# Optimization experiments

Hardware: AMD Instinct MI355X
Metric: run time of the kernel (lower is better)

The kernel has to match this reference:

```python
import jax, jax.numpy as jnp
import numpy as np

C = 1024
HEAD = 128

def setup_inputs() -> dict:
    key = jax.random.key(0)
    kx, kq, kk, kv = jax.random.split(key, 4)
    x = jax.random.normal(kx, (8, 2048, C), dtype=jnp.float32)
    s = 1.0 / np.sqrt(C)
    Wq = jax.random.normal(kq, (C, HEAD), dtype=jnp.float32) * s
    Wk = jax.random.normal(kk, (C, HEAD), dtype=jnp.float32) * s
    Wv = jax.random.normal(kv, (C, HEAD), dtype=jnp.float32) * s
    return {"x": x, "Wq": Wq, "Wk": Wk, "Wv": Wv}

def reference(x, Wq, Wk, Wv):
    B, T, Cdim = x.shape
    q = jnp.einsum('btc,ch->bth', x, Wq)
    k = jnp.einsum('btc,ch->bth', x, Wk)
    v = jnp.einsum('btc,ch->bth', x, Wv)
    # scores scaled by C**-0.5 (faithful to source, which uses input width C)
    wei = jnp.einsum('bqh,bkh->bqk', q, k) * (Cdim ** -0.5)
    causal = jnp.tril(jnp.ones((T, T), dtype=bool))
    wei = jnp.where(causal, wei, -jnp.inf)
    wei = jax.nn.softmax(wei, axis=-1)
    # dropout p=0.0 -> identity
    return jnp.einsum('bqk,bkh->bqh', wei, v)
```

## Files before the change

### kernel.cpp

```cpp
#include <hip/hip_runtime.h>
#include <hip/hip_bf16.h>


typedef __attribute__((ext_vector_type(8))) short bf16x8;
typedef __attribute__((ext_vector_type(4))) float f32x4;

#define NB   8
#define TT   2048
#define CDIM 1024
#define HD   128
#define NTOK (NB * TT)
#define NW   384

using bf16 = __hip_bfloat16;

__device__ __forceinline__ short f2bs(float f) {
    unsigned u = __builtin_bit_cast(unsigned, f);
    return (short)((u + 0x7FFF + ((u >> 16) & 1)) >> 16);
}

__global__ __launch_bounds__(256) void prep_w_kernel(
        const float* __restrict__ Wq, const float* __restrict__ Wk,
        const float* __restrict__ Wv, bf16* __restrict__ Wp) {
    const int f  = blockIdx.x * 256 + threadIdx.x;
    const int l  = f & 63;
    const int nt = (f >> 6) % 24;
    const int sl = f / 1536;
    const int ln = l & 15, quad = l >> 4;
    const int n  = nt * 16 + ln;
    const int w  = n >> 7, h = n & 127;
    const float* W = (w == 0) ? Wq : (w == 1) ? Wk : Wv;
    const int k0 = sl * 32 + quad * 8;
    bf16x8 frag;
    #pragma unroll
    for (int j = 0; j < 8; j++)
        frag[j] = f2bs(W[(long)(k0 + j) * HD + h]);
    *(bf16x8*)((short*)Wp + (long)f * 8) = frag;
}

__global__ __launch_bounds__(512, 4) void qkv_proj_kernel(
        const float* __restrict__ x, const bf16* __restrict__ Wp,
        bf16* __restrict__ Q, bf16* __restrict__ Kp, bf16* __restrict__ Vp) {
    __shared__ __align__(16) short aLDS[2 * 32 * 64 * 8];
    const int tid  = threadIdx.x;
    const int wave = tid >> 6, lane = tid & 63;
    const int quad = lane >> 4, ln = lane & 15;
    const long mbase = (long)blockIdx.x * 32;

    #pragma unroll
    for (int j = 0; j < 8; j++) {
        const int fid = j * 512 + tid;
        const int fl  = fid & 63;
        const int fsl = (fid >> 6) & 31;
        const int fmt = fid >> 11;
        const float4* src = (const float4*)(
            x + (mbase + fmt * 16 + (fl & 15)) * CDIM + fsl * 32 + (fl >> 4) * 8);
        float4 u = src[0], v = src[1];
        bf16x8 fr;
        fr[0] = f2bs(u.x); fr[1] = f2bs(u.y); fr[2] = f2bs(u.z); fr[3] = f2bs(u.w);
        fr[4] = f2bs(v.x); fr[5] = f2bs(v.y); fr[6] = f2bs(v.z); fr[7] = f2bs(v.w);
        *(bf16x8*)(aLDS + (long)fid * 8) = fr;
    }
    __syncthreads();

    const f32x4 zero = {0.f, 0.f, 0.f, 0.f};
    f32x4 acc[2][3];
    #pragma unroll
    for (int mt = 0; mt < 2; mt++)
        #pragma unroll
        for (int nt = 0; nt < 3; nt++) acc[mt][nt] = zero;

    const short* a0 = aLDS + lane * 8;
    const short* bp = (const short*)Wp + (long)wave * 1536 + lane * 8;

    #pragma unroll 4
    for (int sl = 0; sl < 32; sl++) {
        bf16x8 af0 = *(const bf16x8*)(a0 + sl * 512);
        bf16x8 af1 = *(const bf16x8*)(a0 + 16384 + sl * 512);
        bf16x8 b0  = *(const bf16x8*)(bp + (long)sl * 12288);
        bf16x8 b1  = *(const bf16x8*)(bp + (long)sl * 12288 + 512);
        bf16x8 b2  = *(const bf16x8*)(bp + (long)sl * 12288 + 1024);
        acc[0][0] = __builtin_amdgcn_mfma_f32_16x16x32_bf16(af0, b0, acc[0][0], 0, 0, 0);
        acc[0][1] = __builtin_amdgcn_mfma_f32_16x16x32_bf16(af0, b1, acc[0][1], 0, 0, 0);
        acc[0][2] = __builtin_amdgcn_mfma_f32_16x16x32_bf16(af0, b2, acc[0][2], 0, 0, 0);
        acc[1][0] = __builtin_amdgcn_mfma_f32_16x16x32_bf16(af1, b0, acc[1][0], 0, 0, 0);
        acc[1][1] = __builtin_amdgcn_mfma_f32_16x16x32_bf16(af1, b1, acc[1][1], 0, 0, 0);
        acc[1][2] = __builtin_amdgcn_mfma_f32_16x16x32_bf16(af1, b2, acc[1][2], 0, 0, 0);
    }

    __syncthreads();
    short* kT = aLDS;
    short* vT = aLDS + 8192;

    #pragma unroll
    for (int mt = 0; mt < 2; mt++) {
        #pragma unroll
        for (int nt = 0; nt < 3; nt++) {
            const int n = wave * 48 + nt * 16 + ln;
            #pragma unroll
            for (int r = 0; r < 4; r++) {
                const int row = mt * 16 + quad * 4 + r;
                const short hv = f2bs(acc[mt][nt][r]);
                if (n < 128) {
                    long g = mbase + row;
                    int b = (int)(g >> 11), t = (int)(g & (TT - 1));
                    Q[((long)b * TT + t) * HD + n] = __builtin_bit_cast(bf16, hv);
                } else if (n < 256) {
                    kT[row * 136 + (n - 128)] = hv;
                } else {
                    vT[(n - 256) * 40 + row] = hv;
                }
            }
        }
    }
    __syncthreads();

    {
        const long tile = blockIdx.x;
        const int  kc = wave >> 1, ntk = wave & 1;
        bf16x8 kv = *(const bf16x8*)&kT[(ntk*16 + ln)*136 + kc*32 + quad*8];
        *(bf16x8*)((short*)Kp + (tile*8 + wave)*512 + lane*8) = kv;
        bf16x8 vv = *(const bf16x8*)&vT[(wave*16 + ln)*40 + quad*8];
        *(bf16x8*)((short*)Vp + (tile*8 + wave)*512 + lane*8) = vv;
    }
}

__global__ __launch_bounds__(256, 2) void attn_kernel(
        const bf16* __restrict__ Q, const bf16* __restrict__ Kp,
        const bf16* __restrict__ Vp, float* __restrict__ out) {
    __shared__ __align__(16) char smem[33024];

    const int tid  = threadIdx.x;
    const int wave = tid >> 6, lane = tid & 63;
    const int quad = lane >> 4, ln = lane & 15;
    const int b   = blockIdx.x & 7;
    const int idx = blockIdx.x >> 3;
    const int qi  = (idx >> 5) ? (idx & 31) : 63 - (idx & 31);
    const int qb  = qi * 32;
    const int ntiles = qi + 1;
    const int t0 = (ntiles * wave) >> 2;
    const int t1 = (ntiles * (wave + 1)) >> 2;

    const bf16*  Qb  = Q + (long)b * TT * HD;
    const short* Kpb = (const short*)Kp + (long)b * 64 * 4096;
    const short* Vpb = (const short*)Vp + (long)b * 64 * 4096;

    short* pwave = (short*)smem + wave * 2560;

    bf16x8 qf[2][4];
    #pragma unroll
    for (int mt = 0; mt < 2; mt++)
        #pragma unroll
        for (int kc = 0; kc < 4; kc++)
            qf[mt][kc] = *(const bf16x8*)(Qb + (long)(qb + mt*16 + ln)*HD + kc*32 + quad*8);

    const f32x4 zero = {0.f, 0.f, 0.f, 0.f};
    f32x4 o[2][8];
    #pragma unroll
    for (int mt = 0; mt < 2; mt++)
        #pragma unroll
        for (int ht = 0; ht < 8; ht++) o[mt][ht] = zero;
    float li[2][4] = {{0.f,0.f,0.f,0.f},{0.f,0.f,0.f,0.f}};

    for (int kt = t0; kt < t1; ++kt) {
        const int j0 = kt * 32;
        const short* kbase = Kpb + (long)kt * 4096 + lane * 8;
        bf16x8 kf[4][2];
        #pragma unroll
        for (int kc = 0; kc < 4; kc++)
            #pragma unroll
            for (int nt = 0; nt < 2; nt++)
                kf[kc][nt] = *(const bf16x8*)(kbase + (kc*2 + nt)*512);

        f32x4 s[2][2];
        s[0][0] = zero; s[0][1] = zero; s[1][0] = zero; s[1][1] = zero;
        #pragma unroll
        for (int kc = 0; kc < 4; kc++)
            #pragma unroll
            for (int mt = 0; mt < 2; mt++) {
                s[mt][0] = __builtin_amdgcn_mfma_f32_16x16x32_bf16(qf[mt][kc], kf[kc][0], s[mt][0], 0, 0, 0);
                s[mt][1] = __builtin_amdgcn_mfma_f32_16x16x32_bf16(qf[mt][kc], kf[kc][1], s[mt][1], 0, 0, 0);
            }

        short* pb = pwave + (kt & 1) * 1280;
        #pragma unroll
        for (int mt = 0; mt < 2; mt++)
            #pragma unroll
            for (int r = 0; r < 4; r++) {
                const int q = qb + mt*16 + quad*4 + r;
                #pragma unroll
                for (int nt = 0; nt < 2; nt++) {
                    float p = __expf(s[mt][nt][r] * 0.03125f);
                    if (j0 + nt*16 + ln > q) p = 0.f;
                    li[mt][r] += p;
                    pb[(mt*16 + quad*4 + r)*40 + nt*16 + ln] = f2bs(p);
                }
            }

        const short* vbase = Vpb + (long)kt * 4096 + lane * 8;
        bf16x8 vf[8];
        #pragma unroll
        for (int ht = 0; ht < 8; ht++)
            vf[ht] = *(const bf16x8*)(vbase + ht*512);

        bf16x8 pf[2];
        #pragma unroll
        for (int mt = 0; mt < 2; mt++)
            pf[mt] = *(const bf16x8*)&pb[(mt*16 + ln)*40 + quad*8];
        #pragma unroll
        for (int mt = 0; mt < 2; mt++)
            #pragma unroll
            for (int ht = 0; ht < 8; ht++)
                o[mt][ht] = __builtin_amdgcn_mfma_f32_16x16x32_bf16(pf[mt], vf[ht], o[mt][ht], 0, 0, 0);
    }

    #pragma unroll
    for (int mt = 0; mt < 2; mt++)
        #pragma unroll
        for (int r = 0; r < 4; r++)
            #pragma unroll
            for (int d = 1; d < 16; d <<= 1) li[mt][r] += __shfl_xor(li[mt][r], d);

    __syncthreads();
    float* red  = (float*)smem;
    float* redl = (float*)(smem + 32768);
    if (wave & 1) {
        const int slot = wave >> 1;
        #pragma unroll
        for (int mt = 0; mt < 2; mt++)
            #pragma unroll
            for (int ht = 0; ht < 8; ht++)
                #pragma unroll
                for (int r = 0; r < 4; r++)
                    red[slot*4096 + (mt*16 + quad*4 + r)*128 + ht*16 + ln] = o[mt][ht][r];
        if (ln == 0)
            #pragma unroll
            for (int mt = 0; mt < 2; mt++)
                #pragma unroll
                for (int r = 0; r < 4; r++)
                    redl[slot*32 + mt*16 + quad*4 + r] = li[mt][r];
    }
    __syncthreads();
    if (!(wave & 1)) {
        const int slot = wave >> 1;
        #pragma unroll
        for (int mt = 0; mt < 2; mt++) {
            #pragma unroll
            for (int ht = 0; ht < 8; ht++)
                #pragma unroll
                for (int r = 0; r < 4; r++)
                    o[mt][ht][r] += red[slot*4096 + (mt*16 + quad*4 + r)*128 + ht*16 + ln];
            #pragma unroll
            for (int r = 0; r < 4; r++)
                li[mt][r] += redl[slot*32 + mt*16 + quad*4 + r];
        }
    }
    __syncthreads();
    if (wave == 2) {
        #pragma unroll
        for (int mt = 0; mt < 2; mt++) {
            #pragma unroll
            for (int ht = 0; ht < 8; ht++)
                #pragma unroll
                for (int r = 0; r < 4; r++)
                    red[(mt*16 + quad*4 + r)*128 + ht*16 + ln] = o[mt][ht][r];
            if (ln == 0)
                #pragma unroll
                for (int r = 0; r < 4; r++)
                    redl[mt*16 + quad*4 + r] = li[mt][r];
        }
    }
    __syncthreads();
    if (wave == 0) {
        #pragma unroll
        for (int mt = 0; mt < 2; mt++) {
            #pragma unroll
            for (int r = 0; r < 4; r++)
                li[mt][r] += redl[mt*16 + quad*4 + r];
            #pragma unroll
            for (int ht = 0; ht < 8; ht++)
                #pragma unroll
                for (int r = 0; r < 4; r++) {
                    float v = o[mt][ht][r] + red[(mt*16 + quad*4 + r)*128 + ht*16 + ln];
                    out[((long)b*TT + qb + mt*16 + quad*4 + r)*HD + ht*16 + ln] = v / li[mt][r];
                }
        }
    }
}

extern "C" void kernel_launch(void* const* d_in, const int* in_sizes, int n_in,
                              void* d_out, int out_size, void* d_ws, size_t ws_size,
                              hipStream_t stream) {
    const float* x  = (const float*)d_in[0];
    const float* Wq = (const float*)d_in[1];
    const float* Wk = (const float*)d_in[2];
    const float* Wv = (const float*)d_in[3];
    float* outp = (float*)d_out;

    bf16* Wp = (bf16*)d_ws;
    bf16* Qm = Wp + (long)NW * CDIM;
    bf16* Kp = Qm + (long)NTOK * HD;
    bf16* Vp = Kp + (long)NTOK * HD;

    prep_w_kernel<<<192, 256, 0, stream>>>(Wq, Wk, Wv, Wp);
    qkv_proj_kernel<<<512, 512, 0, stream>>>(x, Wp, Qm, Kp, Vp);
    attn_kernel<<<NB * 64, 256, 0, stream>>>(Qm, Kp, Vp, outp);
}
```

Baseline: 143.2 us.

## Double-buffer x tiles in QKV projection with 64-row blocks and swizzled LDS

The QKV projection kernel now handles 64 tokens per block instead of 32, which halves the grid to 256 blocks and doubles reuse of each weight fragment loaded from global memory. Instead of staging the whole 32x1024 x tile up front, it streams x in 128-column chunks through a double-buffered LDS area with an XOR swizzle, prefetching the next chunk into registers while MFMAs run on the current one. This is meant to overlap global loads with compute and cut bank conflicts. The cost is more accumulator registers (occupancy hint lowered to 2), a sync per chunk, and fewer blocks to spread across the CUs.

```diff
diff --git a/kernel.cpp b/kernel.cpp
--- a/kernel.cpp
+++ b/kernel.cpp
@@ -3,6 +3,7 @@
 
 
 typedef __attribute__((ext_vector_type(8))) short bf16x8;
+typedef __attribute__((ext_vector_type(4))) short short4v;
 typedef __attribute__((ext_vector_type(4))) float f32x4;
 
 #define NB   8
@@ -38,62 +39,92 @@
     *(bf16x8*)((short*)Wp + (long)f * 8) = frag;
 }
 
-__global__ __launch_bounds__(512, 4) void qkv_proj_kernel(
+__global__ __launch_bounds__(512, 2) void qkv_proj_kernel(
         const float* __restrict__ x, const bf16* __restrict__ Wp,
         bf16* __restrict__ Q, bf16* __restrict__ Kp, bf16* __restrict__ Vp) {
-    __shared__ __align__(16) short aLDS[2 * 32 * 64 * 8];
+    __shared__ __align__(16) char smem[35840];
     const int tid  = threadIdx.x;
     const int wave = tid >> 6, lane = tid & 63;
     const int quad = lane >> 4, ln = lane & 15;
-    const long mbase = (long)blockIdx.x * 32;
-
-    #pragma unroll
-    for (int j = 0; j < 8; j++) {
-        const int fid = j * 512 + tid;
-        const int fl  = fid & 63;
-        const int fsl = (fid >> 6) & 31;
-        const int fmt = fid >> 11;
-        const float4* src = (const float4*)(
-            x + (mbase + fmt * 16 + (fl & 15)) * CDIM + fsl * 32 + (fl >> 4) * 8);
-        float4 u = src[0], v = src[1];
-        bf16x8 fr;
-        fr[0] = f2bs(u.x); fr[1] = f2bs(u.y); fr[2] = f2bs(u.z); fr[3] = f2bs(u.w);
-        fr[4] = f2bs(v.x); fr[5] = f2bs(v.y); fr[6] = f2bs(v.z); fr[7] = f2bs(v.w);
-        *(bf16x8*)(aLDS + (long)fid * 8) = fr;
-    }
-    __syncthreads();
+    const long mbase = (long)blockIdx.x * 64;
+
+    const float* xrow[4];
+    int woff[4];
+    #pragma unroll
+    for (int k = 0; k < 4; k++) {
+        const int f4 = k * 512 + tid;
+        const int row = f4 >> 5, c16 = f4 & 31;
+        xrow[k] = x + (mbase + row) * CDIM + c16 * 4;
+        woff[k] = (row * 256 + c16 * 8) ^ ((row & 7) << 4);
+    }
+    char* bufs = smem;
+
+    const int xorv = (ln & 7) << 4;
 
     const f32x4 zero = {0.f, 0.f, 0.f, 0.f};
-    f32x4 acc[2][3];
-    #pragma unroll
-    for (int mt = 0; mt < 2; mt++)
+    f32x4 acc[4][3];
+    #pragma unroll
+    for (int mt = 0; mt < 4; mt++)
         #pragma unroll
         for (int nt = 0; nt < 3; nt++) acc[mt][nt] = zero;
 
-    const short* a0 = aLDS + lane * 8;
-    const short* bp = (const short*)Wp + (long)wave * 1536 + lane * 8;
-
-    #pragma unroll 4
-    for (int sl = 0; sl < 32; sl++) {
-        bf16x8 af0 = *(const bf16x8*)(a0 + sl * 512);
-        bf16x8 af1 = *(const bf16x8*)(a0 + 16384 + sl * 512);
-        bf16x8 b0  = *(const bf16x8*)(bp + (long)sl * 12288);
-        bf16x8 b1  = *(const bf16x8*)(bp + (long)sl * 12288 + 512);
-        bf16x8 b2  = *(const bf16x8*)(bp + (long)sl * 12288 + 1024);
-        acc[0][0] = __builtin_amdgcn_mfma_f32_16x16x32_bf16(af0, b0, acc[0][0], 0, 0, 0);
-        acc[0][1] = __builtin_amdgcn_mfma_f32_16x16x32_bf16(af0, b1, acc[0][1], 0, 0, 0);
-        acc[0][2] = __builtin_amdgcn_mfma_f32_16x16x32_bf16(af0, b2, acc[0][2], 0, 0, 0);
-        acc[1][0] = __builtin_amdgcn_mfma_f32_16x16x32_bf16(af1, b0, acc[1][0], 0, 0, 0);
-        acc[1][1] = __builtin_amdgcn_mfma_f32_16x16x32_bf16(af1, b1, acc[1][1], 0, 0, 0);
-        acc[1][2] = __builtin_amdgcn_mfma_f32_16x16x32_bf16(af1, b2, acc[1][2], 0, 0, 0);
-    }
-
-    __syncthreads();
-    short* kT = aLDS;
-    short* vT = aLDS + 8192;
-
-    #pragma unroll
-    for (int mt = 0; mt < 2; mt++) {
+    const short* bps = (const short*)Wp + (long)wave * 1536 + lane * 8;
+
+    {
+        float4 xn[4];
+        #pragma unroll
+        for (int k = 0; k < 4; k++) xn[k] = *(const float4*)(xrow[k]);
+        #pragma unroll
+        for (int k = 0; k < 4; k++) {
+            short4v v = { f2bs(xn[k].x), f2bs(xn[k].y), f2bs(xn[k].z), f2bs(xn[k].w) };
+            *(short4v*)(bufs + woff[k]) = v;
+        }
+    }
+    __syncthreads();
+
+    int cur = 0;
+    for (int c = 0; c < 8; ++c) {
+        float4 xn[4];
+        if (c + 1 < 8) {
+            #pragma unroll
+            for (int k = 0; k < 4; k++)
+                xn[k] = *(const float4*)(xrow[k] + (c + 1) * 128);
+        }
+        const char* bb = bufs + cur * 16384;
+        #pragma unroll
+        for (int slc = 0; slc < 4; ++slc) {
+            const int sg = c * 4 + slc;
+            bf16x8 b0 = *(const bf16x8*)(bps + (long)sg * 12288);
+            bf16x8 b1 = *(const bf16x8*)(bps + (long)sg * 12288 + 512);
+            bf16x8 b2 = *(const bf16x8*)(bps + (long)sg * 12288 + 1024);
+            const int cb = (slc * 64 + quad * 16) ^ xorv;
+            bf16x8 af[4];
+            #pragma unroll
+            for (int mt = 0; mt < 4; mt++)
+                af[mt] = *(const bf16x8*)(bb + (mt * 16 + ln) * 256 + cb);
+            #pragma unroll
+            for (int mt = 0; mt < 4; mt++) {
+                acc[mt][0] = __builtin_amdgcn_mfma_f32_16x16x32_bf16(af[mt], b0, acc[mt][0], 0, 0, 0);
+                acc[mt][1] = __builtin_amdgcn_mfma_f32_16x16x32_bf16(af[mt], b1, acc[mt][1], 0, 0, 0);
+                acc[mt][2] = __builtin_amdgcn_mfma_f32_16x16x32_bf16(af[mt], b2, acc[mt][2], 0, 0, 0);
+            }
+        }
+        if (c + 1 < 8) {
+            char* bn = bufs + (cur ^ 1) * 16384;
+            #pragma unroll
+            for (int k = 0; k < 4; k++) {
+                short4v v = { f2bs(xn[k].x), f2bs(xn[k].y), f2bs(xn[k].z), f2bs(xn[k].w) };
+                *(short4v*)(bn + woff[k]) = v;
+            }
+        }
+        __syncthreads();
+        cur ^= 1;
+    }
+
+    short* kT = (short*)smem;
+    short* vT = (short*)smem + 8704;
+    #pragma unroll
+    for (int mt = 0; mt < 4; mt++) {
         #pragma unroll
         for (int nt = 0; nt < 3; nt++) {
             const int n = wave * 48 + nt * 16 + ln;
@@ -108,19 +139,20 @@
                 } else if (n < 256) {
                     kT[row * 136 + (n - 128)] = hv;
                 } else {
-                    vT[(n - 256) * 40 + row] = hv;
+                    vT[(n - 256) * 72 + row] = hv;
                 }
             }
         }
     }
     __syncthreads();
 
-    {
-        const long tile = blockIdx.x;
+    #pragma unroll
+    for (int tt = 0; tt < 2; tt++) {
+        const long tile = (long)blockIdx.x * 2 + tt;
         const int  kc = wave >> 1, ntk = wave & 1;
-        bf16x8 kv = *(const bf16x8*)&kT[(ntk*16 + ln)*136 + kc*32 + quad*8];
+        bf16x8 kv = *(const bf16x8*)&kT[(tt*32 + ntk*16 + ln)*136 + kc*32 + quad*8];
         *(bf16x8*)((short*)Kp + (tile*8 + wave)*512 + lane*8) = kv;
-        bf16x8 vv = *(const bf16x8*)&vT[(wave*16 + ln)*40 + quad*8];
+        bf16x8 vv = *(const bf16x8*)&vT[(wave*16 + ln)*72 + tt*32 + quad*8];
         *(bf16x8*)((short*)Vp + (tile*8 + wave)*512 + lane*8) = vv;
     }
 }
@@ -303,6 +335,6 @@
     bf16* Vp = Kp + (long)NTOK * HD;
 
     prep_w_kernel<<<192, 256, 0, stream>>>(Wq, Wk, Wv, Wp);
-    qkv_proj_kernel<<<512, 512, 0, stream>>>(x, Wp, Qm, Kp, Vp);
+    qkv_proj_kernel<<<256, 512, 0, stream>>>(x, Wp, Qm, Kp, Vp);
     attn_kernel<<<NB * 64, 256, 0, stream>>>(Qm, Kp, Vp, outp);
 }
```

After: 154.2 us. +7.7%, slower.

## Double-buffer x tile loads in QKV projection to overlap with MFMA

Applied to the files above, without the earlier changes.

The QKV projection kernel used to load and convert the whole 32x1024 x tile into LDS before any MFMA work. It now splits the K dimension into four stages and double-buffers 16KB LDS halves, issuing the next stage's global loads before the current stage's MFMAs and converting them afterwards. This hides global-load latency behind compute and halves the LDS footprint (64KB to 32KB), which may allow more resident blocks. The cost is extra barriers per stage and more live registers holding the prefetched data.

```diff
diff --git a/kernel.cpp b/kernel.cpp
--- a/kernel.cpp
+++ b/kernel.cpp
@@ -41,27 +41,18 @@
 __global__ __launch_bounds__(512, 4) void qkv_proj_kernel(
         const float* __restrict__ x, const bf16* __restrict__ Wp,
         bf16* __restrict__ Q, bf16* __restrict__ Kp, bf16* __restrict__ Vp) {
-    __shared__ __align__(16) short aLDS[2 * 32 * 64 * 8];
+    __shared__ __align__(16) char smem[32768];
     const int tid  = threadIdx.x;
     const int wave = tid >> 6, lane = tid & 63;
     const int quad = lane >> 4, ln = lane & 15;
     const long mbase = (long)blockIdx.x * 32;
 
-    #pragma unroll
-    for (int j = 0; j < 8; j++) {
-        const int fid = j * 512 + tid;
-        const int fl  = fid & 63;
-        const int fsl = (fid >> 6) & 31;
-        const int fmt = fid >> 11;
-        const float4* src = (const float4*)(
-            x + (mbase + fmt * 16 + (fl & 15)) * CDIM + fsl * 32 + (fl >> 4) * 8);
-        float4 u = src[0], v = src[1];
-        bf16x8 fr;
-        fr[0] = f2bs(u.x); fr[1] = f2bs(u.y); fr[2] = f2bs(u.z); fr[3] = f2bs(u.w);
-        fr[4] = f2bs(v.x); fr[5] = f2bs(v.y); fr[6] = f2bs(v.z); fr[7] = f2bs(v.w);
-        *(bf16x8*)(aLDS + (long)fid * 8) = fr;
-    }
-    __syncthreads();
+    const int fl = tid & 63;
+    const float* src0 = x + (mbase + ((tid >> 6) & 1) * 16 + (fl & 15)) * CDIM
+                          + (tid >> 7) * 32 + (fl >> 4) * 8;
+    const float* src1 = x + (mbase + (((tid + 512) >> 6) & 1) * 16 + (fl & 15)) * CDIM
+                          + ((tid + 512) >> 7) * 32 + (fl >> 4) * 8;
+    char* bufs = smem;
 
     const f32x4 zero = {0.f, 0.f, 0.f, 0.f};
     f32x4 acc[2][3];
@@ -70,28 +61,62 @@
         #pragma unroll
         for (int nt = 0; nt < 3; nt++) acc[mt][nt] = zero;
 
-    const short* a0 = aLDS + lane * 8;
-    const short* bp = (const short*)Wp + (long)wave * 1536 + lane * 8;
-
-    #pragma unroll 4
-    for (int sl = 0; sl < 32; sl++) {
-        bf16x8 af0 = *(const bf16x8*)(a0 + sl * 512);
-        bf16x8 af1 = *(const bf16x8*)(a0 + 16384 + sl * 512);
-        bf16x8 b0  = *(const bf16x8*)(bp + (long)sl * 12288);
-        bf16x8 b1  = *(const bf16x8*)(bp + (long)sl * 12288 + 512);
-        bf16x8 b2  = *(const bf16x8*)(bp + (long)sl * 12288 + 1024);
-        acc[0][0] = __builtin_amdgcn_mfma_f32_16x16x32_bf16(af0, b0, acc[0][0], 0, 0, 0);
-        acc[0][1] = __builtin_amdgcn_mfma_f32_16x16x32_bf16(af0, b1, acc[0][1], 0, 0, 0);
-        acc[0][2] = __builtin_amdgcn_mfma_f32_16x16x32_bf16(af0, b2, acc[0][2], 0, 0, 0);
-        acc[1][0] = __builtin_amdgcn_mfma_f32_16x16x32_bf16(af1, b0, acc[1][0], 0, 0, 0);
-        acc[1][1] = __builtin_amdgcn_mfma_f32_16x16x32_bf16(af1, b1, acc[1][1], 0, 0, 0);
-        acc[1][2] = __builtin_amdgcn_mfma_f32_16x16x32_bf16(af1, b2, acc[1][2], 0, 0, 0);
-    }
-
-    __syncthreads();
-    short* kT = aLDS;
-    short* vT = aLDS + 8192;
-
+    const short* bps = (const short*)Wp + (long)wave * 1536 + lane * 8;
+
+    {
+        float4 a0 = *(const float4*)(src0);
+        float4 a1 = *(const float4*)(src0 + 4);
+        float4 c0 = *(const float4*)(src1);
+        float4 c1 = *(const float4*)(src1 + 4);
+        bf16x8 fA, fB;
+        fA[0]=f2bs(a0.x); fA[1]=f2bs(a0.y); fA[2]=f2bs(a0.z); fA[3]=f2bs(a0.w);
+        fA[4]=f2bs(a1.x); fA[5]=f2bs(a1.y); fA[6]=f2bs(a1.z); fA[7]=f2bs(a1.w);
+        fB[0]=f2bs(c0.x); fB[1]=f2bs(c0.y); fB[2]=f2bs(c0.z); fB[3]=f2bs(c0.w);
+        fB[4]=f2bs(c1.x); fB[5]=f2bs(c1.y); fB[6]=f2bs(c1.z); fB[7]=f2bs(c1.w);
+        *(bf16x8*)(bufs + tid * 16) = fA;
+        *(bf16x8*)(bufs + tid * 16 + 8192) = fB;
+    }
+    __syncthreads();
+
+    for (int g = 0; g < 4; ++g) {
+        float4 a0, a1, c0, c1;
+        if (g < 3) {
+            const float* p0 = src0 + (g + 1) * 256;
+            const float* p1 = src1 + (g + 1) * 256;
+            a0 = *(const float4*)(p0);  a1 = *(const float4*)(p0 + 4);
+            c0 = *(const float4*)(p1);  c1 = *(const float4*)(p1 + 4);
+        }
+        const char* bb = bufs + (g & 1) * 16384;
+        #pragma unroll
+        for (int s = 0; s < 8; ++s) {
+            const int sg = g * 8 + s;
+            bf16x8 b0 = *(const bf16x8*)(bps + (long)sg * 12288);
+            bf16x8 b1 = *(const bf16x8*)(bps + (long)sg * 12288 + 512);
+            bf16x8 b2 = *(const bf16x8*)(bps + (long)sg * 12288 + 1024);
+            bf16x8 af0 = *(const bf16x8*)(bb + s * 2048 + lane * 16);
+            bf16x8 af1 = *(const bf16x8*)(bb + s * 2048 + 1024 + lane * 16);
+            acc[0][0] = __builtin_amdgcn_mfma_f32_16x16x32_bf16(af0, b0, acc[0][0], 0, 0, 0);
+            acc[0][1] = __builtin_amdgcn_mfma_f32_16x16x32_bf16(af0, b1, acc[0][1], 0, 0, 0);
+            acc[0][2] = __builtin_amdgcn_mfma_f32_16x16x32_bf16(af0, b2, acc[0][2], 0, 0, 0);
+            acc[1][0] = __builtin_amdgcn_mfma_f32_16x16x32_bf16(af1, b0, acc[1][0], 0, 0, 0);
+            acc[1][1] = __builtin_amdgcn_mfma_f32_16x16x32_bf16(af1, b1, acc[1][1], 0, 0, 0);
+            acc[1][2] = __builtin_amdgcn_mfma_f32_16x16x32_bf16(af1, b2, acc[1][2], 0, 0, 0);
+        }
+        if (g < 3) {
+            char* bn = bufs + ((g + 1) & 1) * 16384;
+            bf16x8 fA, fB;
+            fA[0]=f2bs(a0.x); fA[1]=f2bs(a0.y); fA[2]=f2bs(a0.z); fA[3]=f2bs(a0.w);
+            fA[4]=f2bs(a1.x); fA[5]=f2bs(a1.y); fA[6]=f2bs(a1.z); fA[7]=f2bs(a1.w);
+            fB[0]=f2bs(c0.x); fB[1]=f2bs(c0.y); fB[2]=f2bs(c0.z); fB[3]=f2bs(c0.w);
+            fB[4]=f2bs(c1.x); fB[5]=f2bs(c1.y); fB[6]=f2bs(c1.z); fB[7]=f2bs(c1.w);
+            *(bf16x8*)(bn + tid * 16) = fA;
+            *(bf16x8*)(bn + tid * 16 + 8192) = fB;
+        }
+        __syncthreads();
+    }
+
+    short* kT = (short*)smem;
+    short* vT = (short*)smem + 8192;
     #pragma unroll
     for (int mt = 0; mt < 2; mt++) {
         #pragma unroll
@@ -102,8 +127,8 @@
                 const int row = mt * 16 + quad * 4 + r;
                 const short hv = f2bs(acc[mt][nt][r]);
                 if (n < 128) {
-                    long g = mbase + row;
-                    int b = (int)(g >> 11), t = (int)(g & (TT - 1));
+                    long gg = mbase + row;
+                    int b = (int)(gg >> 11), t = (int)(gg & (TT - 1));
                     Q[((long)b * TT + t) * HD + n] = __builtin_bit_cast(bf16, hv);
                 } else if (n < 256) {
                     kT[row * 136 + (n - 128)] = hv;
```

Measured after the change: 150.8 us. 1.05x slower.
